# Kernel tuning notes

Hardware: AMD Instinct MI355X
Metric: run time of the kernel (lower is better)

Reference implementation:

```python
import jax, jax.numpy as jnp
import numpy as np

TOPK = 8
NUM_SEM = 32


def _forward(x, sem_w, sem_b, q_w, k_w, v_w, fuse_w, fuse_b, alpha, ln_gamma, ln_beta):
    B, C, H, W = x.shape
    N = H * W
    xf = x.reshape(B, C, N)

    # semantic soft-assignment (softmax over K regions per position)
    sem_logits = jnp.einsum('kc,bcn->bkn', sem_w, xf) + sem_b[None, :, None]
    sem = jax.nn.softmax(sem_logits, axis=1)
    sem = jnp.nan_to_num(sem, posinf=1e-6, neginf=0.0)

    # 1x1 conv projections as GEMMs
    q = jnp.einsum('dc,bcn->bdn', q_w, xf)   # (B,d,N)
    k = jnp.einsum('dc,bcn->bdn', k_w, xf)   # (B,d,N)
    v = jnp.einsum('oc,bcn->bon', v_w, xf)   # (B,C,N)
    d = q.shape[1]
    scale = d ** 0.5 + 1e-6

    # --- dense semantic-region attention branch ---
    region_k = jnp.einsum('bkn,bdn->bkd', sem, k)
    region_v = jnp.einsum('bkn,bcn->bkc', sem, v)
    attn_region = jax.nn.softmax(jnp.einsum('bdn,bkd->bkn', q, region_k) / scale, axis=1)
    attn_region = jnp.nan_to_num(attn_region, posinf=1e6, neginf=-1e6)
    cont_out = jnp.einsum('bkn,bkc->bcn', attn_region, region_v)
    cont_out = jnp.nan_to_num(cont_out, posinf=1e6, neginf=-1e6)

    # --- sparse top-k gather attention branch ---
    M = min(256, N)
    _, ti = jax.lax.top_k(jax.lax.stop_gradient(sem), M)       # (B,K,M) top positions per region
    hr = jnp.argmax(sem, axis=1)                                # (B,N) hard region per position
    idx_pp = jnp.take_along_axis(ti, hr[:, :, None], axis=1)    # (B,N,M) pool indices for each position

    bidx = jnp.arange(B)[:, None, None]
    qt = jnp.swapaxes(q, 1, 2)  # (B,N,d)
    kt = jnp.swapaxes(k, 1, 2)  # (B,N,d)
    vt = jnp.swapaxes(v, 1, 2)  # (B,N,C)

    kg = kt[bidx, idx_pp]                                       # (B,N,M,d) gathered key pool
    sims = jnp.einsum('bnd,bnmd->bnm', qt, kg) / scale          # (B,N,M)
    kn = min(TOPK, M)
    topv, topi = jax.lax.top_k(sims, kn)                        # (B,N,kn)
    att = jax.nn.softmax(topv, axis=-1)
    actual = jnp.take_along_axis(idx_pp, topi, axis=2)          # (B,N,kn) spatial indices
    vg = vt[bidx, actual]                                       # (B,N,kn,C)
    sparse_out = jnp.swapaxes(jnp.einsum('bnt,bntc->bnc', att, vg), 1, 2)  # (B,C,N)
    sparse_out = jnp.nan_to_num(sparse_out, posinf=1e6, neginf=-1e6)

    # --- combine, fuse, residual, channel LayerNorm ---
    a = jax.nn.sigmoid(alpha)
    combined = a * cont_out + (1.0 - a) * sparse_out
    combined = jnp.nan_to_num(combined, posinf=1e6, neginf=-1e6)
    fused = jnp.einsum('oc,bcn->bon', fuse_w, combined) + fuse_b[None, :, None]
    out = x + fused.reshape(B, C, H, W)

    xp = out.transpose(0, 2, 3, 1)  # (B,H,W,C)
    mu = xp.mean(-1, keepdims=True)
    var = xp.var(-1, keepdims=True)
    xp = (xp - mu) / jnp.sqrt(var + 1e-5) * ln_gamma + ln_beta
    return xp.transpose(0, 3, 1, 2)


def setup_inputs() -> dict:
    key = jax.random.key(0)
    ks = jax.random.split(key, 8)
    B, C, H, W = 2, 256, 64, 64
    d = C // 4  # reduction=4
    Ksem = NUM_SEM
    f32 = jnp.float32
    return {
        'x': jax.random.normal(ks[0], (B, C, H, W), f32),
        'sem_w': jax.random.normal(ks[1], (Ksem, C), f32) * 0.05,
        'sem_b': jnp.zeros((Ksem,), f32),
        'q_w': jax.random.normal(ks[2], (d, C), f32) * (2.0 / C) ** 0.5,
        'k_w': jax.random.normal(ks[3], (d, C), f32) * (2.0 / C) ** 0.5,
        'v_w': jax.random.normal(ks[4], (C, C), f32) * (2.0 / C) ** 0.5,
        'fuse_w': jax.random.normal(ks[5], (C, C), f32) * (1.0 / C) ** 0.5,
        'fuse_b': jnp.zeros((C,), f32),
        'alpha': jnp.float32(0.5),
        'ln_gamma': jnp.ones((C,), f32),
        'ln_beta': jnp.zeros((C,), f32),
    }


def reference(x, sem_w, sem_b, q_w, k_w, v_w, fuse_w, fuse_b, alpha, ln_gamma, ln_beta):
    return _forward(x, sem_w, sem_b, q_w, k_w, v_w, fuse_w, fuse_b, alpha, ln_gamma, ln_beta)
```

## Files before the change

### kernel.cpp

```cpp
#include <hip/hip_runtime.h>
#include <math.h>

#define QOFF 32
#define KOFF 96
#define VOFF 160

__global__ __launch_bounds__(256) void proj_kernel(
    const float* __restrict__ x,
    const float* __restrict__ sem_w, const float* __restrict__ sem_b,
    const float* __restrict__ q_w, const float* __restrict__ k_w,
    const float* __restrict__ v_w, float* __restrict__ Y)
{
    const int t = threadIdx.x;
    const int n0 = blockIdx.x * 64;
    const int oc0 = blockIdx.y * 64;
    const int b = blockIdx.z;
    const int ty = t >> 4, tx = t & 15;

    __shared__ float As[16][68];
    __shared__ float Bs[16][64];

    float acc[4][4];
#pragma unroll
    for (int i = 0; i < 4; i++)
#pragma unroll
        for (int j = 0; j < 4; j++) acc[i][j] = 0.f;

    const int oc_l = t >> 2;
    const int cp = t & 3;
    const int oc_g = oc0 + oc_l;
    const float* wrow = nullptr;
    if (oc_g < 32) wrow = sem_w + oc_g * 256;
    else if (oc_g < 96) wrow = q_w + (oc_g - 32) * 256;
    else if (oc_g < 160) wrow = k_w + (oc_g - 96) * 256;
    else if (oc_g < 416) wrow = v_w + (oc_g - 160) * 256;

    const int bk = t >> 4;
    const int bn = (t & 15) << 2;

    for (int c0 = 0; c0 < 256; c0 += 16) {
        __syncthreads();
        float4 w4 = make_float4(0.f, 0.f, 0.f, 0.f);
        if (wrow) w4 = *(const float4*)(wrow + c0 + (cp << 2));
        As[(cp << 2) + 0][oc_l] = w4.x;
        As[(cp << 2) + 1][oc_l] = w4.y;
        As[(cp << 2) + 2][oc_l] = w4.z;
        As[(cp << 2) + 3][oc_l] = w4.w;
        *(float4*)&Bs[bk][bn] =
            *(const float4*)(x + ((size_t)(b * 256 + c0 + bk)) * 4096 + n0 + bn);
        __syncthreads();
#pragma unroll
        for (int kk = 0; kk < 16; kk++) {
            float4 a4 = *(float4*)&As[kk][ty << 2];
            float4 b4 = *(float4*)&Bs[kk][tx << 2];
            acc[0][0] += a4.x * b4.x; acc[0][1] += a4.x * b4.y;
            acc[0][2] += a4.x * b4.z; acc[0][3] += a4.x * b4.w;
            acc[1][0] += a4.y * b4.x; acc[1][1] += a4.y * b4.y;
            acc[1][2] += a4.y * b4.z; acc[1][3] += a4.y * b4.w;
            acc[2][0] += a4.z * b4.x; acc[2][1] += a4.z * b4.y;
            acc[2][2] += a4.z * b4.z; acc[2][3] += a4.z * b4.w;
            acc[3][0] += a4.w * b4.x; acc[3][1] += a4.w * b4.y;
            acc[3][2] += a4.w * b4.z; acc[3][3] += a4.w * b4.w;
        }
    }

    if (oc0 + (ty << 2) < 416) {
        float bias[4];
#pragma unroll
        for (int i = 0; i < 4; i++) {
            int oc = oc0 + (ty << 2) + i;
            bias[i] = (oc < 32) ? sem_b[oc] : 0.f;
        }
#pragma unroll
        for (int j = 0; j < 4; j++) {
            int n = n0 + (tx << 2) + j;
            float4 o4 = make_float4(acc[0][j] + bias[0], acc[1][j] + bias[1],
                                    acc[2][j] + bias[2], acc[3][j] + bias[3]);
            *(float4*)(Y + ((size_t)(b * 4096 + n)) * 416 + oc0 + (ty << 2)) = o4;
        }
    }
}

__global__ __launch_bounds__(256) void semsoft_kernel(float* __restrict__ Y,
                                                      int* __restrict__ hr)
{
    const int g = blockIdx.x * 256 + threadIdx.x;
    float* row = Y + (size_t)g * 416;
    float v[32];
#pragma unroll
    for (int i = 0; i < 8; i++) *(float4*)&v[i * 4] = *(float4*)&row[i * 4];
    float mx = v[0]; int am = 0;
#pragma unroll
    for (int kk = 1; kk < 32; kk++) if (v[kk] > mx) { mx = v[kk]; am = kk; }
    float s = 0.f;
#pragma unroll
    for (int kk = 0; kk < 32; kk++) { v[kk] = expf(v[kk] - mx); s += v[kk]; }
    const float inv = 1.f / s;
#pragma unroll
    for (int kk = 0; kk < 32; kk++) v[kk] *= inv;
#pragma unroll
    for (int i = 0; i < 8; i++) *(float4*)&row[i * 4] = *(float4*)&v[i * 4];
    hr[g] = am;
}

__global__ __launch_bounds__(256) void region_partial_kernel(
    const float* __restrict__ Y, float* __restrict__ P)
{
    const int ch = blockIdx.x, b = blockIdx.y;
    const int t = threadIdx.x;
    __shared__ float row_s[416];
    const int kset = t & 7;
    const int dds = t >> 3;
    float acc[4][10];
#pragma unroll
    for (int i = 0; i < 4; i++)
#pragma unroll
        for (int j = 0; j < 10; j++) acc[i][j] = 0.f;
    const size_t gbase = (size_t)(b * 4096 + ch * 128);
    for (int nn = 0; nn < 128; nn++) {
        __syncthreads();
        const float* row = Y + (gbase + nn) * 416;
        if (t < 208) { row_s[t] = row[t]; row_s[t + 208] = row[t + 208]; }
        __syncthreads();
        float sv[4], kv[10];
#pragma unroll
        for (int i = 0; i < 4; i++) sv[i] = row_s[(kset << 2) + i];
#pragma unroll
        for (int j = 0; j < 10; j++) kv[j] = row_s[96 + dds * 10 + j];
#pragma unroll
        for (int i = 0; i < 4; i++)
#pragma unroll
            for (int j = 0; j < 10; j++) acc[i][j] += sv[i] * kv[j];
    }
    float* Pb = P + ((size_t)(b * 32 + ch)) * 10240;
#pragma unroll
    for (int i = 0; i < 4; i++)
#pragma unroll
        for (int j = 0; j < 10; j++)
            Pb[((kset << 2) + i) * 320 + dds * 10 + j] = acc[i][j];
}

__global__ __launch_bounds__(256) void region_reduce_kernel(
    const float* __restrict__ P, float* __restrict__ region)
{
    const int idx = blockIdx.x * 256 + threadIdx.x;
    if (idx >= 2 * 10240) return;
    const int b = idx / 10240, rem = idx - b * 10240;
    float s = 0.f;
    for (int ch = 0; ch < 32; ch++)
        s += P[((size_t)(b * 32 + ch)) * 10240 + rem];
    region[(size_t)b * 10240 + rem] = s;
}

__global__ __launch_bounds__(256) void topk_sem_kernel(
    const float* __restrict__ Y, int* __restrict__ ti)
{
    const int kreg = blockIdx.x, b = blockIdx.y;
    const int t = threadIdx.x;
    __shared__ int wpart[4];
    __shared__ int sh_eq[256];
    __shared__ int ctr;

    unsigned int uv[16];
    const int nbase = t * 16;
#pragma unroll
    for (int i = 0; i < 16; i++) {
        float v = Y[((size_t)(b * 4096 + nbase + i)) * 416 + kreg];
        unsigned int u = __float_as_uint(v);
        uv[i] = (u & 0x80000000u) ? ~u : (u | 0x80000000u);
    }
    unsigned long long lo = 0ull, hi = 0xFFFFFFFFull;
    while (lo < hi) {
        const unsigned int mid = (unsigned int)((lo + hi + 1ull) >> 1);
        int c = 0;
#pragma unroll
        for (int i = 0; i < 16; i++) c += (uv[i] >= mid) ? 1 : 0;
#pragma unroll
        for (int off = 1; off < 64; off <<= 1) c += __shfl_xor(c, off);
        __syncthreads();
        if ((t & 63) == 0) wpart[t >> 6] = c;
        __syncthreads();
        const int tot = wpart[0] + wpart[1] + wpart[2] + wpart[3];
        if (tot >= 256) lo = mid; else hi = (unsigned long long)mid - 1ull;
    }
    const unsigned int T = (unsigned int)lo;
    int cgt = 0, ceq = 0;
#pragma unroll
    for (int i = 0; i < 16; i++) { cgt += (uv[i] > T) ? 1 : 0; ceq += (uv[i] == T) ? 1 : 0; }
    int cg = cgt;
#pragma unroll
    for (int off = 1; off < 64; off <<= 1) cg += __shfl_xor(cg, off);
    __syncthreads();
    if ((t & 63) == 0) wpart[t >> 6] = cg;
    sh_eq[t] = ceq;
    if (t == 0) ctr = 0;
    __syncthreads();
    const int c1 = wpart[0] + wpart[1] + wpart[2] + wpart[3];
    int eqbase = 0;
    for (int i = 0; i < t; i++) eqbase += sh_eq[i];
    int* outp = ti + ((size_t)(b * 32 + kreg)) * 256;
    int seen = 0;
#pragma unroll
    for (int i = 0; i < 16; i++) {
        if (uv[i] > T) {
            int pos = atomicAdd(&ctr, 1);
            outp[pos] = nbase + i;
        } else if (uv[i] == T) {
            int r = eqbase + seen; seen++;
            if (c1 + r < 256) outp[c1 + r] = nbase + i;
        }
    }
}

__global__ __launch_bounds__(256) void sparse_attn_kernel(
    const float* __restrict__ Y, const int* __restrict__ hr,
    const int* __restrict__ ti, float* __restrict__ sp)
{
    const int t = threadIdx.x;
    const int wid = t >> 6, lane = t & 63;
    const int g = blockIdx.x * 4 + wid;
    const int b = g >> 12;
    __shared__ float q_s[4][64];
    __shared__ int pool_s[4][256];
    __shared__ float sims_s[4][256];

    q_s[wid][lane] = Y[(size_t)g * 416 + QOFF + lane];
    const int region = hr[g];
    *(int4*)&pool_s[wid][lane << 2] =
        *(const int4*)(ti + ((size_t)(b * 32 + region)) * 256 + (lane << 2));
    __syncthreads();

    float4 qr[16];
    {
        const float4* q4 = (const float4*)q_s[wid];
#pragma unroll
        for (int j = 0; j < 16; j++) qr[j] = q4[j];
    }
    const float inv_scale = 1.0f / (8.0f + 1e-6f);
#pragma unroll
    for (int r = 0; r < 4; r++) {
        const int m = (r << 6) + lane;
        const int kidx = pool_s[wid][m];
        const float4* kr = (const float4*)(Y + ((size_t)(b * 4096 + kidx)) * 416 + KOFF);
        float s = 0.f;
#pragma unroll
        for (int j = 0; j < 16; j++) {
            float4 kv = kr[j];
            s += qr[j].x * kv.x + qr[j].y * kv.y + qr[j].z * kv.z + qr[j].w * kv.w;
        }
        sims_s[wid][m] = s * inv_scale;
    }
    __syncthreads();

    float topv[8]; int topm[8];
#pragma unroll
    for (int sel = 0; sel < 8; sel++) {
        float4 sv = *(float4*)&sims_s[wid][lane << 2];
        float bv = sv.x; int bm = (lane << 2);
        if (sv.y > bv) { bv = sv.y; bm = (lane << 2) + 1; }
        if (sv.z > bv) { bv = sv.z; bm = (lane << 2) + 2; }
        if (sv.w > bv) { bv = sv.w; bm = (lane << 2) + 3; }
#pragma unroll
        for (int off = 1; off < 64; off <<= 1) {
            float ov = __shfl_xor(bv, off);
            int om = __shfl_xor(bm, off);
            if (ov > bv || (ov == bv && om < bm)) { bv = ov; bm = om; }
        }
        topv[sel] = bv; topm[sel] = bm;
        if (lane == (bm >> 2)) sims_s[wid][bm] = -3e38f;
        __syncthreads();
    }

    const float mx = topv[0];
    float att[8]; float esum = 0.f;
#pragma unroll
    for (int j = 0; j < 8; j++) { att[j] = expf(topv[j] - mx); esum += att[j]; }
    const float inv = 1.f / esum;

    float4 acc = make_float4(0.f, 0.f, 0.f, 0.f);
#pragma unroll
    for (int j = 0; j < 8; j++) {
        const int actual = pool_s[wid][topm[j]];
        const float4 vv = *(const float4*)(
            Y + ((size_t)(b * 4096 + actual)) * 416 + VOFF + (lane << 2));
        const float w = att[j] * inv;
        acc.x += w * vv.x; acc.y += w * vv.y; acc.z += w * vv.z; acc.w += w * vv.w;
    }
    *(float4*)(sp + (size_t)g * 256 + (lane << 2)) = acc;
}

__global__ __launch_bounds__(256) void combine_kernel(
    const float* __restrict__ Y, const float* __restrict__ region,
    const float* __restrict__ alpha, float* __restrict__ sp)
{
    const int t = threadIdx.x;
    const int wid = t >> 6, lane = t & 63;
    const int g = blockIdx.x * 4 + wid;
    const int b = g >> 12;
    __shared__ float rk_s[32][65];
    __shared__ float rv_s[32][256];
    __shared__ float a_s[4][32];
    __shared__ float q_s[4][64];

    const float* reg = region + (size_t)b * 10240;
    for (int idx = t; idx < 10240; idx += 256) {
        const int kk = idx / 320, dd = idx - kk * 320;
        const float v = reg[idx];
        if (dd < 64) rk_s[kk][dd] = v; else rv_s[kk][dd - 64] = v;
    }
    q_s[wid][lane] = Y[(size_t)g * 416 + QOFF + lane];
    __syncthreads();

    const int kk = lane & 31, half = lane >> 5;
    float part = 0.f;
    {
        const float* qsw = q_s[wid] + (half << 5);
        const float* rkr = &rk_s[kk][half << 5];
#pragma unroll
        for (int j = 0; j < 32; j++) part += qsw[j] * rkr[j];
    }
    part += __shfl_xor(part, 32);
    const float inv_scale = 1.0f / (8.0f + 1e-6f);
    const float logit = part * inv_scale;
    float mx = logit;
#pragma unroll
    for (int off = 1; off < 32; off <<= 1) mx = fmaxf(mx, __shfl_xor(mx, off));
    const float e = expf(logit - mx);
    float s = e;
#pragma unroll
    for (int off = 1; off < 32; off <<= 1) s += __shfl_xor(s, off);
    if (half == 0) a_s[wid][kk] = e / s;
    __syncthreads();

    float4 acc = make_float4(0.f, 0.f, 0.f, 0.f);
#pragma unroll
    for (int k2 = 0; k2 < 32; k2++) {
        const float w = a_s[wid][k2];
        const float4 rv = *(const float4*)&rv_s[k2][lane << 2];
        acc.x += w * rv.x; acc.y += w * rv.y; acc.z += w * rv.z; acc.w += w * rv.w;
    }
    const float asig = 1.f / (1.f + expf(-alpha[0]));
    float* spr = sp + (size_t)g * 256 + (lane << 2);
    float4 spv = *(float4*)spr;
    float4 o;
    o.x = asig * acc.x + (1.f - asig) * spv.x;
    o.y = asig * acc.y + (1.f - asig) * spv.y;
    o.z = asig * acc.z + (1.f - asig) * spv.z;
    o.w = asig * acc.w + (1.f - asig) * spv.w;
    *(float4*)spr = o;
}

__global__ __launch_bounds__(256) void fuse_ln_kernel(
    const float* __restrict__ comb, const float* __restrict__ fuse_w,
    const float* __restrict__ fuse_b, const float* __restrict__ x,
    const float* __restrict__ ln_g, const float* __restrict__ ln_b,
    float* __restrict__ out)
{
    const int t = threadIdx.x;
    const int n0 = blockIdx.x << 5;
    const int b = blockIdx.y;

    __shared__ float smem[32 * 256 + 32 * 36];
    float (*Ws)[256] = (float (*)[256])smem;
    float (*cs)[36] = (float (*)[36])(smem + 32 * 256);
    float (*Fs)[260] = (float (*)[260])smem;
    __shared__ float red1[8][32], red2[8][32];
    __shared__ float mu_s[32], rs_s[32];

    const int og = t & 63;
    const int ng = t >> 6;
    float acc[4][8];
#pragma unroll
    for (int i = 0; i < 4; i++)
#pragma unroll
        for (int j = 0; j < 8; j++) acc[i][j] = 0.f;

    const int cl = (t << 2) & 31;
    const int nl = t >> 3;

    for (int c0 = 0; c0 < 256; c0 += 32) {
        __syncthreads();
        {
            const float* wr = fuse_w + (size_t)t * 256 + c0;
#pragma unroll
            for (int j = 0; j < 8; j++) {
                float4 w4 = *(const float4*)(wr + (j << 2));
                Ws[(j << 2) + 0][t] = w4.x;
                Ws[(j << 2) + 1][t] = w4.y;
                Ws[(j << 2) + 2][t] = w4.z;
                Ws[(j << 2) + 3][t] = w4.w;
            }
        }
        {
            float4 c4 = *(const float4*)(
                comb + ((size_t)(b * 4096 + n0 + nl)) * 256 + c0 + cl);
            cs[cl + 0][nl] = c4.x;
            cs[cl + 1][nl] = c4.y;
            cs[cl + 2][nl] = c4.z;
            cs[cl + 3][nl] = c4.w;
        }
        __syncthreads();
#pragma unroll
        for (int cc = 0; cc < 32; cc++) {
            float4 w4 = *(float4*)&Ws[cc][og << 2];
            float4 ca = *(float4*)&cs[cc][ng << 3];
            float4 cb = *(float4*)&cs[cc][(ng << 3) + 4];
            float wv[4] = {w4.x, w4.y, w4.z, w4.w};
            float cv[8] = {ca.x, ca.y, ca.z, ca.w, cb.x, cb.y, cb.z, cb.w};
#pragma unroll
            for (int i = 0; i < 4; i++)
#pragma unroll
                for (int j = 0; j < 8; j++) acc[i][j] += wv[i] * cv[j];
        }
    }

    __syncthreads();
#pragma unroll
    for (int i = 0; i < 4; i++) {
        const int o = (og << 2) + i;
        const float fb = fuse_b[o];
        const float* xr = x + ((size_t)(b * 256 + o)) * 4096 + n0 + (ng << 3);
        float4 xa = *(const float4*)xr;
        float4 xb = *(const float4*)(xr + 4);
        float xv[8] = {xa.x, xa.y, xa.z, xa.w, xb.x, xb.y, xb.z, xb.w};
#pragma unroll
        for (int j = 0; j < 8; j++)
            Fs[(ng << 3) + j][o] = acc[i][j] + fb + xv[j];
    }
    __syncthreads();
    {
        const int n = t & 31, part = t >> 5;
        float s1 = 0.f, s2 = 0.f;
#pragma unroll
        for (int i = 0; i < 32; i++) {
            const float v = Fs[n][(part << 5) + i];
            s1 += v; s2 += v * v;
        }
        red1[part][n] = s1; red2[part][n] = s2;
    }
    __syncthreads();
    if (t < 32) {
        float s1 = 0.f, s2 = 0.f;
#pragma unroll
        for (int p = 0; p < 8; p++) { s1 += red1[p][t]; s2 += red2[p][t]; }
        const float mean = s1 * (1.f / 256.f);
        const float var = s2 * (1.f / 256.f) - mean * mean;
        mu_s[t] = mean;
        rs_s[t] = rsqrtf(var + 1e-5f);
    }
    __syncthreads();
#pragma unroll
    for (int j = 0; j < 32; j++) {
        const int idx = (j << 8) + t;
        const int o = idx >> 5, n = idx & 31;
        const float v = (Fs[n][o] - mu_s[n]) * rs_s[n] * ln_g[o] + ln_b[o];
        out[((size_t)(b * 256 + o)) * 4096 + n0 + n] = v;
    }
}

extern "C" void kernel_launch(void* const* d_in, const int* in_sizes, int n_in,
                              void* d_out, int out_size, void* d_ws, size_t ws_size,
                              hipStream_t stream)
{
    const float* x = (const float*)d_in[0];
    const float* sem_w = (const float*)d_in[1];
    const float* sem_b = (const float*)d_in[2];
    const float* q_w = (const float*)d_in[3];
    const float* k_w = (const float*)d_in[4];
    const float* v_w = (const float*)d_in[5];
    const float* fuse_w = (const float*)d_in[6];
    const float* fuse_b = (const float*)d_in[7];
    const float* alpha = (const float*)d_in[8];
    const float* ln_g = (const float*)d_in[9];
    const float* ln_b = (const float*)d_in[10];
    float* out = (float*)d_out;

    char* ws = (char*)d_ws;
    float* Y   = (float*)(ws);
    float* SP  = (float*)(ws + 13631488);
    float* P   = (float*)(ws + 22020096);
    float* REG = (float*)(ws + 24641536);
    int*   HR  = (int*)  (ws + 24723456);
    int*   TI  = (int*)  (ws + 24756224);

    proj_kernel<<<dim3(64, 7, 2), 256, 0, stream>>>(x, sem_w, sem_b, q_w, k_w, v_w, Y);
    semsoft_kernel<<<32, 256, 0, stream>>>(Y, HR);
    region_partial_kernel<<<dim3(32, 2), 256, 0, stream>>>(Y, P);
    region_reduce_kernel<<<80, 256, 0, stream>>>(P, REG);
    topk_sem_kernel<<<dim3(32, 2), 256, 0, stream>>>(Y, TI);
    sparse_attn_kernel<<<2048, 256, 0, stream>>>(Y, HR, TI, SP);
    combine_kernel<<<2048, 256, 0, stream>>>(Y, REG, alpha, SP);
    fuse_ln_kernel<<<dim3(128, 2), 256, 0, stream>>>(SP, fuse_w, fuse_b, x, ln_g, ln_b, out);
}
```

Before: 369.7 us.

## Bin positions by hard region to share key-pool tiles in sparse attention

A new bin kernel groups positions by their hard-assigned region using atomic counters. Sparse attention now runs one block group per region and stages that region's 256-key pool in shared memory once per pass, then scores 16 query positions against it. Previously each position gathered the whole pool from global memory on its own. The region-partial reduction now stages 8 rows per sync, and the combine kernel processes 32 positions per block while reusing the loaded region tensors. The costs are an extra memset and binning launch, plus possible load imbalance when some regions own many more positions than others.

```diff
diff --git a/kernel.cpp b/kernel.cpp
--- a/kernel.cpp
+++ b/kernel.cpp
@@ -4,6 +4,7 @@
 #define QOFF 32
 #define KOFF 96
 #define VOFF 160
+#define NSUB 8
 
 __global__ __launch_bounds__(256) void proj_kernel(
     const float* __restrict__ x,
@@ -103,12 +104,22 @@
     hr[g] = am;
 }
 
+__global__ __launch_bounds__(256) void bin_kernel(
+    const int* __restrict__ hr, int* __restrict__ cnt, int* __restrict__ plist)
+{
+    const int g = blockIdx.x * 256 + threadIdx.x;
+    const int b = g >> 12, n = g & 4095;
+    const int r = hr[g];
+    const int slot = atomicAdd(&cnt[b * 32 + r], 1);
+    plist[((size_t)(b * 32 + r)) * 4096 + slot] = n;
+}
+
 __global__ __launch_bounds__(256) void region_partial_kernel(
     const float* __restrict__ Y, float* __restrict__ P)
 {
     const int ch = blockIdx.x, b = blockIdx.y;
     const int t = threadIdx.x;
-    __shared__ float row_s[416];
+    __shared__ float row_s[8][420];
     const int kset = t & 7;
     const int dds = t >> 3;
     float acc[4][10];
@@ -117,20 +128,27 @@
 #pragma unroll
         for (int j = 0; j < 10; j++) acc[i][j] = 0.f;
     const size_t gbase = (size_t)(b * 4096 + ch * 128);
-    for (int nn = 0; nn < 128; nn++) {
-        __syncthreads();
-        const float* row = Y + (gbase + nn) * 416;
-        if (t < 208) { row_s[t] = row[t]; row_s[t + 208] = row[t + 208]; }
-        __syncthreads();
-        float sv[4], kv[10];
-#pragma unroll
-        for (int i = 0; i < 4; i++) sv[i] = row_s[(kset << 2) + i];
-#pragma unroll
-        for (int j = 0; j < 10; j++) kv[j] = row_s[96 + dds * 10 + j];
-#pragma unroll
-        for (int i = 0; i < 4; i++)
-#pragma unroll
-            for (int j = 0; j < 10; j++) acc[i][j] += sv[i] * kv[j];
+    for (int r0 = 0; r0 < 128; r0 += 8) {
+        __syncthreads();
+#pragma unroll
+        for (int r = 0; r < 8; r++) {
+            const float* rp = Y + (gbase + r0 + r) * 416;
+            row_s[r][t] = rp[t];
+            if (t < 160) row_s[r][t + 256] = rp[t + 256];
+        }
+        __syncthreads();
+#pragma unroll
+        for (int r = 0; r < 8; r++) {
+            float sv[4], kv[10];
+#pragma unroll
+            for (int i = 0; i < 4; i++) sv[i] = row_s[r][(kset << 2) + i];
+#pragma unroll
+            for (int j = 0; j < 10; j++) kv[j] = row_s[r][96 + dds * 10 + j];
+#pragma unroll
+            for (int i = 0; i < 4; i++)
+#pragma unroll
+                for (int j = 0; j < 10; j++) acc[i][j] += sv[i] * kv[j];
+        }
     }
     float* Pb = P + ((size_t)(b * 32 + ch)) * 10240;
 #pragma unroll
@@ -213,94 +231,138 @@
 }
 
 __global__ __launch_bounds__(256) void sparse_attn_kernel(
-    const float* __restrict__ Y, const int* __restrict__ hr,
-    const int* __restrict__ ti, float* __restrict__ sp)
-{
-    const int t = threadIdx.x;
-    const int wid = t >> 6, lane = t & 63;
-    const int g = blockIdx.x * 4 + wid;
-    const int b = g >> 12;
-    __shared__ float q_s[4][64];
-    __shared__ int pool_s[4][256];
-    __shared__ float sims_s[4][256];
-
-    q_s[wid][lane] = Y[(size_t)g * 416 + QOFF + lane];
-    const int region = hr[g];
-    *(int4*)&pool_s[wid][lane << 2] =
-        *(const int4*)(ti + ((size_t)(b * 32 + region)) * 256 + (lane << 2));
-    __syncthreads();
-
-    float4 qr[16];
-    {
-        const float4* q4 = (const float4*)q_s[wid];
-#pragma unroll
-        for (int j = 0; j < 16; j++) qr[j] = q4[j];
-    }
+    const float* __restrict__ Y, const int* __restrict__ cnt,
+    const int* __restrict__ plist, const int* __restrict__ ti,
+    float* __restrict__ sp)
+{
+    const int rb = blockIdx.x;
+    const int sub = blockIdx.y;
+    const int b = rb >> 5;
+    const int t = threadIdx.x, wid = t >> 6, lane = t & 63;
+
+    const int count = cnt[rb];
+    const int chunk = (count + NSUB - 1) / NSUB;
+    const int p0 = sub * chunk;
+    const int p1 = min(p0 + chunk, count);
+    if (p1 <= p0) return;
+    const int npass = (p1 - p0 + 15) >> 4;
+
+    __shared__ int pool_s[256];
+    __shared__ float K_sT[64][128];
+    __shared__ float q_sT[4][64][4];
+    __shared__ float sims_s[4][4][256];
+
+    if (t < 64)
+        *(int4*)&pool_s[t << 2] = *(const int4*)(ti + (size_t)rb * 256 + (t << 2));
+    __syncthreads();
+
     const float inv_scale = 1.0f / (8.0f + 1e-6f);
-#pragma unroll
-    for (int r = 0; r < 4; r++) {
-        const int m = (r << 6) + lane;
-        const int kidx = pool_s[wid][m];
-        const float4* kr = (const float4*)(Y + ((size_t)(b * 4096 + kidx)) * 416 + KOFF);
-        float s = 0.f;
-#pragma unroll
-        for (int j = 0; j < 16; j++) {
-            float4 kv = kr[j];
-            s += qr[j].x * kv.x + qr[j].y * kv.y + qr[j].z * kv.z + qr[j].w * kv.w;
-        }
-        sims_s[wid][m] = s * inv_scale;
-    }
-    __syncthreads();
-
-    float topv[8]; int topm[8];
-#pragma unroll
-    for (int sel = 0; sel < 8; sel++) {
-        float4 sv = *(float4*)&sims_s[wid][lane << 2];
-        float bv = sv.x; int bm = (lane << 2);
-        if (sv.y > bv) { bv = sv.y; bm = (lane << 2) + 1; }
-        if (sv.z > bv) { bv = sv.z; bm = (lane << 2) + 2; }
-        if (sv.w > bv) { bv = sv.w; bm = (lane << 2) + 3; }
-#pragma unroll
-        for (int off = 1; off < 64; off <<= 1) {
-            float ov = __shfl_xor(bv, off);
-            int om = __shfl_xor(bm, off);
-            if (ov > bv || (ov == bv && om < bm)) { bv = ov; bm = om; }
-        }
-        topv[sel] = bv; topm[sel] = bm;
-        if (lane == (bm >> 2)) sims_s[wid][bm] = -3e38f;
-        __syncthreads();
-    }
-
-    const float mx = topv[0];
-    float att[8]; float esum = 0.f;
-#pragma unroll
-    for (int j = 0; j < 8; j++) { att[j] = expf(topv[j] - mx); esum += att[j]; }
-    const float inv = 1.f / esum;
-
-    float4 acc = make_float4(0.f, 0.f, 0.f, 0.f);
-#pragma unroll
-    for (int j = 0; j < 8; j++) {
-        const int actual = pool_s[wid][topm[j]];
-        const float4 vv = *(const float4*)(
-            Y + ((size_t)(b * 4096 + actual)) * 416 + VOFF + (lane << 2));
-        const float w = att[j] * inv;
-        acc.x += w * vv.x; acc.y += w * vv.y; acc.z += w * vv.z; acc.w += w * vv.w;
-    }
-    *(float4*)(sp + (size_t)g * 256 + (lane << 2)) = acc;
+    const int* myplist = plist + (size_t)rb * 4096;
+    const int krow = t >> 1;
+    const int jh = t & 1;
+
+    for (int pass = 0; pass < npass; pass++) {
+        int gg[4]; bool val[4];
+#pragma unroll
+        for (int p = 0; p < 4; p++) {
+            const int idx = p0 + (pass << 4) + (wid << 2) + p;
+            val[p] = (idx < p1);
+            const int n = myplist[val[p] ? idx : p0];
+            gg[p] = (b << 12) + n;
+            q_sT[wid][lane][p] = Y[(size_t)gg[p] * 416 + QOFF + lane];
+        }
+
+        for (int half = 0; half < 2; half++) {
+            __syncthreads();
+            {
+                const int kidx = pool_s[(half << 7) + krow];
+                const float* kr = Y + ((size_t)((b << 12) + kidx)) * 416 + KOFF + (jh << 5);
+#pragma unroll
+                for (int jj = 0; jj < 8; jj++) {
+                    float4 kv = *(const float4*)(kr + (jj << 2));
+                    const int jb = (jh << 5) + (jj << 2);
+                    K_sT[jb + 0][krow] = kv.x;
+                    K_sT[jb + 1][krow] = kv.y;
+                    K_sT[jb + 2][krow] = kv.z;
+                    K_sT[jb + 3][krow] = kv.w;
+                }
+            }
+            __syncthreads();
+            float a00 = 0.f, a01 = 0.f, a10 = 0.f, a11 = 0.f;
+            float a20 = 0.f, a21 = 0.f, a30 = 0.f, a31 = 0.f;
+#pragma unroll
+            for (int j = 0; j < 64; j++) {
+                const float2 kv = *(const float2*)&K_sT[j][lane << 1];
+                const float4 q4 = *(const float4*)&q_sT[wid][j][0];
+                a00 += q4.x * kv.x; a01 += q4.x * kv.y;
+                a10 += q4.y * kv.x; a11 += q4.y * kv.y;
+                a20 += q4.z * kv.x; a21 += q4.z * kv.y;
+                a30 += q4.w * kv.x; a31 += q4.w * kv.y;
+            }
+            const int sbase = (half << 7) + (lane << 1);
+            *(float2*)&sims_s[wid][0][sbase] = make_float2(a00 * inv_scale, a01 * inv_scale);
+            *(float2*)&sims_s[wid][1][sbase] = make_float2(a10 * inv_scale, a11 * inv_scale);
+            *(float2*)&sims_s[wid][2][sbase] = make_float2(a20 * inv_scale, a21 * inv_scale);
+            *(float2*)&sims_s[wid][3][sbase] = make_float2(a30 * inv_scale, a31 * inv_scale);
+        }
+        asm volatile("s_waitcnt lgkmcnt(0)" ::: "memory");
+
+#pragma unroll
+        for (int p = 0; p < 4; p++) {
+            if (!val[p]) continue;
+            float4 sv = *(const float4*)&sims_s[wid][p][lane << 2];
+            float s0 = sv.x, s1 = sv.y, s2 = sv.z, s3 = sv.w;
+            float topv[8]; int topm[8];
+#pragma unroll
+            for (int sel = 0; sel < 8; sel++) {
+                float bv = s0; int bm = (lane << 2);
+                if (s1 > bv) { bv = s1; bm = (lane << 2) + 1; }
+                if (s2 > bv) { bv = s2; bm = (lane << 2) + 2; }
+                if (s3 > bv) { bv = s3; bm = (lane << 2) + 3; }
+#pragma unroll
+                for (int off = 1; off < 64; off <<= 1) {
+                    const float ov = __shfl_xor(bv, off);
+                    const int om = __shfl_xor(bm, off);
+                    if (ov > bv || (ov == bv && om < bm)) { bv = ov; bm = om; }
+                }
+                topv[sel] = bv; topm[sel] = bm;
+                const bool own = (lane == (bm >> 2));
+                const int sl = bm & 3;
+                s0 = (own && sl == 0) ? -3e38f : s0;
+                s1 = (own && sl == 1) ? -3e38f : s1;
+                s2 = (own && sl == 2) ? -3e38f : s2;
+                s3 = (own && sl == 3) ? -3e38f : s3;
+            }
+            const float mx = topv[0];
+            float att[8]; float esum = 0.f;
+#pragma unroll
+            for (int j = 0; j < 8; j++) { att[j] = expf(topv[j] - mx); esum += att[j]; }
+            const float inv = 1.f / esum;
+            float4 acc = make_float4(0.f, 0.f, 0.f, 0.f);
+#pragma unroll
+            for (int j = 0; j < 8; j++) {
+                const int actual = pool_s[topm[j]];
+                const float4 vv = *(const float4*)(
+                    Y + ((size_t)((b << 12) + actual)) * 416 + VOFF + (lane << 2));
+                const float w = att[j] * inv;
+                acc.x += w * vv.x; acc.y += w * vv.y;
+                acc.z += w * vv.z; acc.w += w * vv.w;
+            }
+            *(float4*)(sp + (size_t)gg[p] * 256 + (lane << 2)) = acc;
+        }
+    }
 }
 
 __global__ __launch_bounds__(256) void combine_kernel(
     const float* __restrict__ Y, const float* __restrict__ region,
     const float* __restrict__ alpha, float* __restrict__ sp)
 {
-    const int t = threadIdx.x;
-    const int wid = t >> 6, lane = t & 63;
-    const int g = blockIdx.x * 4 + wid;
-    const int b = g >> 12;
+    const int t = threadIdx.x, wid = t >> 6, lane = t & 63;
+    const int b = blockIdx.y;
+    const int n0 = blockIdx.x << 5;
     __shared__ float rk_s[32][65];
     __shared__ float rv_s[32][256];
-    __shared__ float a_s[4][32];
-    __shared__ float q_s[4][64];
+    __shared__ float q_all[32][64];
 
     const float* reg = region + (size_t)b * 10240;
     for (int idx = t; idx < 10240; idx += 256) {
@@ -308,46 +370,53 @@
         const float v = reg[idx];
         if (dd < 64) rk_s[kk][dd] = v; else rv_s[kk][dd - 64] = v;
     }
-    q_s[wid][lane] = Y[(size_t)g * 416 + QOFF + lane];
-    __syncthreads();
-
+    const size_t g0 = (size_t)(b << 12) + n0;
+    for (int idx = t; idx < 2048; idx += 256)
+        q_all[idx >> 6][idx & 63] = Y[(g0 + (idx >> 6)) * 416 + QOFF + (idx & 63)];
+    __syncthreads();
+
+    const float asig = 1.f / (1.f + expf(-alpha[0]));
+    const float inv_scale = 1.0f / (8.0f + 1e-6f);
     const int kk = lane & 31, half = lane >> 5;
-    float part = 0.f;
-    {
-        const float* qsw = q_s[wid] + (half << 5);
-        const float* rkr = &rk_s[kk][half << 5];
-#pragma unroll
-        for (int j = 0; j < 32; j++) part += qsw[j] * rkr[j];
-    }
-    part += __shfl_xor(part, 32);
-    const float inv_scale = 1.0f / (8.0f + 1e-6f);
-    const float logit = part * inv_scale;
-    float mx = logit;
-#pragma unroll
-    for (int off = 1; off < 32; off <<= 1) mx = fmaxf(mx, __shfl_xor(mx, off));
-    const float e = expf(logit - mx);
-    float s = e;
-#pragma unroll
-    for (int off = 1; off < 32; off <<= 1) s += __shfl_xor(s, off);
-    if (half == 0) a_s[wid][kk] = e / s;
-    __syncthreads();
-
-    float4 acc = make_float4(0.f, 0.f, 0.f, 0.f);
-#pragma unroll
-    for (int k2 = 0; k2 < 32; k2++) {
-        const float w = a_s[wid][k2];
-        const float4 rv = *(const float4*)&rv_s[k2][lane << 2];
-        acc.x += w * rv.x; acc.y += w * rv.y; acc.z += w * rv.z; acc.w += w * rv.w;
-    }
-    const float asig = 1.f / (1.f + expf(-alpha[0]));
-    float* spr = sp + (size_t)g * 256 + (lane << 2);
-    float4 spv = *(float4*)spr;
-    float4 o;
-    o.x = asig * acc.x + (1.f - asig) * spv.x;
-    o.y = asig * acc.y + (1.f - asig) * spv.y;
-    o.z = asig * acc.z + (1.f - asig) * spv.z;
-    o.w = asig * acc.w + (1.f - asig) * spv.w;
-    *(float4*)spr = o;
+
+    for (int pp = 0; pp < 8; pp++) {
+        const int n_l = (wid << 3) + pp;
+        const size_t g = g0 + n_l;
+        float part = 0.f;
+        {
+            const float* qr = &q_all[n_l][half << 5];
+            const float* rkr = &rk_s[kk][half << 5];
+#pragma unroll
+            for (int j = 0; j < 32; j++) part += qr[j] * rkr[j];
+        }
+        part += __shfl_xor(part, 32);
+        const float logit = part * inv_scale;
+        float mx = logit;
+#pragma unroll
+        for (int off = 1; off < 32; off <<= 1) mx = fmaxf(mx, __shfl_xor(mx, off));
+        const float e = expf(logit - mx);
+        float s = e;
+#pragma unroll
+        for (int off = 1; off < 32; off <<= 1) s += __shfl_xor(s, off);
+        const float w_own = e / s;
+
+        float4 acc = make_float4(0.f, 0.f, 0.f, 0.f);
+#pragma unroll
+        for (int k2 = 0; k2 < 32; k2++) {
+            const float w = __shfl(w_own, k2);
+            const float4 rv = *(const float4*)&rv_s[k2][lane << 2];
+            acc.x += w * rv.x; acc.y += w * rv.y;
+            acc.z += w * rv.z; acc.w += w * rv.w;
+        }
+        float* spr = sp + g * 256 + (lane << 2);
+        float4 spv = *(float4*)spr;
+        float4 o;
+        o.x = asig * acc.x + (1.f - asig) * spv.x;
+        o.y = asig * acc.y + (1.f - asig) * spv.y;
+        o.z = asig * acc.z + (1.f - asig) * spv.z;
+        o.w = asig * acc.w + (1.f - asig) * spv.w;
+        *(float4*)spr = o;
+    }
 }
 
 __global__ __launch_bounds__(256) void fuse_ln_kernel(
@@ -476,19 +545,23 @@
     float* out = (float*)d_out;
 
     char* ws = (char*)d_ws;
-    float* Y   = (float*)(ws);
-    float* SP  = (float*)(ws + 13631488);
-    float* P   = (float*)(ws + 22020096);
-    float* REG = (float*)(ws + 24641536);
-    int*   HR  = (int*)  (ws + 24723456);
-    int*   TI  = (int*)  (ws + 24756224);
+    float* Y    = (float*)(ws);
+    float* SP   = (float*)(ws + 13631488);
+    float* P    = (float*)(ws + 22020096);
+    float* REG  = (float*)(ws + 24641536);
+    int*   HR   = (int*)  (ws + 24723456);
+    int*   TI   = (int*)  (ws + 24756224);
+    int*   CNT  = (int*)  (ws + 24821760);
+    int*   PLIST= (int*)  (ws + 24822016);
 
     proj_kernel<<<dim3(64, 7, 2), 256, 0, stream>>>(x, sem_w, sem_b, q_w, k_w, v_w, Y);
     semsoft_kernel<<<32, 256, 0, stream>>>(Y, HR);
+    hipMemsetAsync(CNT, 0, 256, stream);
+    bin_kernel<<<32, 256, 0, stream>>>(HR, CNT, PLIST);
     region_partial_kernel<<<dim3(32, 2), 256, 0, stream>>>(Y, P);
     region_reduce_kernel<<<80, 256, 0, stream>>>(P, REG);
     topk_sem_kernel<<<dim3(32, 2), 256, 0, stream>>>(Y, TI);
-    sparse_attn_kernel<<<2048, 256, 0, stream>>>(Y, HR, TI, SP);
-    combine_kernel<<<2048, 256, 0, stream>>>(Y, REG, alpha, SP);
+    sparse_attn_kernel<<<dim3(64, NSUB), 256, 0, stream>>>(Y, CNT, PLIST, TI, SP);
+    combine_kernel<<<dim3(128, 2), 256, 0, stream>>>(Y, REG, alpha, SP);
     fuse_ln_kernel<<<dim3(128, 2), 256, 0, stream>>>(SP, fuse_w, fuse_b, x, ln_g, ln_b, out);
 }
```

After: 331.6 us. 10.3% less time.
